# Kernel optimization log

Hardware: AMD Instinct MI355X
Metric: run time of the kernel (lower is better)

## Reference

```python
import math
import jax, jax.numpy as jnp
import numpy as np

# MrLoRA ranks: halving from highest_rank = total_rank//2 = 32 down to 1
RANKS = [32, 16, 8, 4, 2, 1]
TOTAL_R = sum(RANKS)  # 63
LORA_ALPHA = 16.0
IN_F, OUT_F = 4096, 4096
BATCH, SEQ = 4, 2048


def setup_inputs() -> dict:
    key = jax.random.key(0)
    k0, k1, k2, k3 = jax.random.split(key, 4)
    x = jax.random.normal(k0, (BATCH, SEQ, IN_F), dtype=jnp.float32)
    # Base linear layer (nn.Linear weight is [out, in], plus bias)
    W_base = jax.random.normal(k1, (OUT_F, IN_F), dtype=jnp.float32) * 0.02
    b_base = jnp.zeros((OUT_F,), dtype=jnp.float32)
    # Concatenated per-rank LoRA weights: A rows stacked -> [TOTAL_R, IN_F],
    # B cols stacked -> [OUT_F, TOTAL_R]. Mathematically identical to the
    # per-rank ModuleDict since the branch outputs are summed.
    A = jax.random.normal(k2, (TOTAL_R, IN_F), dtype=jnp.float32) / math.sqrt(IN_F)
    B = jax.random.normal(k3, (OUT_F, TOTAL_R), dtype=jnp.float32) * 0.02
    alphas = jnp.ones((len(RANKS),), dtype=jnp.float32)
    # use_rslora=True -> scaling = alpha / sqrt(r)
    scalings = jnp.array([LORA_ALPHA / math.sqrt(r) for r in RANKS], dtype=jnp.float32)
    return {"x": x, "W_base": W_base, "b_base": b_base, "A": A, "B": B,
            "alphas": alphas, "scalings": scalings}


def reference(x, W_base, b_base, A, B, alphas, scalings):
    # static map: row r of concatenated A belongs to which rank branch
    seg = np.repeat(np.arange(len(RANKS)), RANKS)  # [TOTAL_R]
    base = jnp.einsum('bsi,oi->bso', x, W_base) + b_base
    # dropout p=0 -> identity
    combined = (alphas * scalings)[seg]            # [TOTAL_R]
    z = jnp.einsum('bsi,ri->bsr', x, A) * combined # scaled low-rank projections
    adapter = jnp.einsum('bsr,or->bso', z, B)      # sum over all rank branches
    return base + adapter
```

## Files before the change

### kernel.cpp

```cpp
#include <hip/hip_runtime.h>
#include <hip/hip_fp16.h>
#include <cstdint>

#define IN_F 4096
#define OUT_F 4096
#define M_TOT 8192
#define TOTAL_R 63

typedef __attribute__((ext_vector_type(8))) _Float16 f16x8;
typedef __attribute__((ext_vector_type(4))) float f32x4;
typedef __attribute__((ext_vector_type(8))) unsigned short u16x8;
typedef __attribute__((ext_vector_type(4))) unsigned short u16x4;

__device__ __forceinline__ void gload_lds16(const void* g, void* l) {
  __builtin_amdgcn_global_load_lds((const __attribute__((address_space(1))) void*)g,
                                   (__attribute__((address_space(3))) void*)l,
                                   16, 0, 0);
}

__device__ __forceinline__ int seg_of(int r) {
  return (r < 32) ? 0 : (r < 48) ? 1 : (r < 56) ? 2 : (r < 60) ? 3 : (r < 62) ? 4 : 5;
}

__global__ void conv_x_f16(const float* __restrict__ x, uint16_t* __restrict__ xh) {
  size_t i = (size_t)blockIdx.x * blockDim.x + threadIdx.x;
  const float4* xv = (const float4*)x;
  float4 v0 = xv[2 * i];
  float4 v1 = xv[2 * i + 1];
  float v[8] = {v0.x, v0.y, v0.z, v0.w, v1.x, v1.y, v1.z, v1.w};
  u16x8 h;
#pragma unroll
  for (int k = 0; k < 8; ++k) h[k] = __half_as_ushort(__float2half_rn(v[k]));
  *(u16x8*)(xh + 8 * i) = h;
}

__global__ __launch_bounds__(256) void merge_w_kernel(
    const float* __restrict__ Wb, const float* __restrict__ A,
    const float* __restrict__ Bm, const float* __restrict__ alphas,
    const float* __restrict__ scalings, uint16_t* __restrict__ wh) {
  __shared__ float sA[63 * 256];
  __shared__ float sBT[63 * 64];
  const int t = threadIdx.x;
  const int bo = blockIdx.x >> 4, bi = blockIdx.x & 15;
  const int o0 = bo * 64, i0 = bi * 256;
  const int wv = t >> 6, ln = t & 63;

#pragma unroll
  for (int k = 0; k < 16; ++k) {
    int r = k * 4 + wv;
    if (r < 63) {
      f32x4 v = *(const f32x4*)(A + (size_t)r * IN_F + i0 + ln * 4);
      *(f32x4*)(sA + r * 256 + ln * 4) = v;
    }
  }
  {
    const int oo = ln;
    const int rbase = wv * 16;
#pragma unroll
    for (int rr = 0; rr < 16; ++rr) {
      int r = rbase + rr;
      if (r < 63) {
        int s = seg_of(r);
        sBT[r * 64 + oo] = Bm[(size_t)(o0 + oo) * TOTAL_R + r] * alphas[s] * scalings[s];
      }
    }
  }
  __syncthreads();

  const int oo = t & 63, iq = t >> 6;
  const size_t obase = (size_t)(o0 + oo) * IN_F + i0 + iq * 64;
  f32x4 acc4[16];
#pragma unroll
  for (int v = 0; v < 16; ++v) acc4[v] = *(const f32x4*)(Wb + obase + v * 4);
#pragma unroll 9
  for (int r = 0; r < 63; ++r) {
    const float coeff = sBT[r * 64 + oo];
    const f32x4* ar = (const f32x4*)(sA + r * 256 + iq * 64);
#pragma unroll
    for (int v = 0; v < 16; ++v) acc4[v] += coeff * ar[v];
  }
#pragma unroll
  for (int v = 0; v < 16; ++v) {
    u16x4 h;
#pragma unroll
    for (int k = 0; k < 4; ++k) h[k] = __half_as_ushort(__float2half_rn(acc4[v][k]));
    *(u16x4*)(wh + obase + v * 4) = h;
  }
}

__global__ __launch_bounds__(256, 2) void gemm_mrlora(
    const uint16_t* __restrict__ xh, const uint16_t* __restrict__ wh,
    const float* __restrict__ bias, float* __restrict__ out) {
  __shared__ uint16_t sX[8192];
  __shared__ uint16_t sW[4096];
  const int t = threadIdx.x;
  const int l = t & 63;
  const int w = t >> 6;
  const int wr = w >> 1, wc = w & 1;
  const int lr = l & 15, lg = l >> 4;

  const int xcd = blockIdx.x & 7;
  const int kk = blockIdx.x >> 3;
  const int bm = xcd * 4 + (kk & 3);
  const int bn = kk >> 2;
  const size_t brow = (size_t)bm * 256;
  const size_t bcol = (size_t)bn * 128;

  const int lrow = t >> 3;
  const int sp = (t & 7) ^ (lrow & 7);
  const int grow = lrow * 2 + (sp >> 2);
  const int gcol = (sp & 3) * 8;
  const uint16_t* pX = xh + (brow + grow) * (size_t)IN_F + gcol;
  const uint16_t* pW = wh + (bcol + grow) * (size_t)IN_F + gcol;
  const int t8 = t * 8;

  int aoff[8], boff[4];
#pragma unroll
  for (int i = 0; i < 8; ++i) {
    int row = wr * 128 + i * 16 + lr;
    aoff[i] = (row >> 1) * 64 + (((((row & 1) << 2) | lg) ^ ((row >> 1) & 7)) << 3);
  }
#pragma unroll
  for (int j = 0; j < 4; ++j) {
    int row = wc * 64 + j * 16 + lr;
    boff[j] = (row >> 1) * 64 + (((((row & 1) << 2) | lg) ^ ((row >> 1) & 7)) << 3);
  }

  f32x4 acc[8][4] = {};

  for (int kt = 0; kt < IN_F / 32; ++kt) {
    const int k0 = kt * 32;
#pragma unroll
    for (int g = 0; g < 4; ++g)
      gload_lds16(pX + (size_t)(64 * g) * IN_F + k0, &sX[t8 + g * 2048]);
#pragma unroll
    for (int g = 0; g < 2; ++g)
      gload_lds16(pW + (size_t)(64 * g) * IN_F + k0, &sW[t8 + g * 2048]);
    __syncthreads();

    f16x8 af[8], bf[4];
#pragma unroll
    for (int i = 0; i < 8; ++i) af[i] = *(const f16x8*)&sX[aoff[i]];
#pragma unroll
    for (int j = 0; j < 4; ++j) bf[j] = *(const f16x8*)&sW[boff[j]];

#pragma unroll
    for (int i = 0; i < 8; ++i)
#pragma unroll
      for (int j = 0; j < 4; ++j)
        acc[i][j] = __builtin_amdgcn_mfma_f32_16x16x32_f16(af[i], bf[j], acc[i][j], 0, 0, 0);

    __syncthreads();
  }

#pragma unroll
  for (int j = 0; j < 4; ++j) {
    const size_t col = bcol + wc * 64 + j * 16 + lr;
    const float bs = bias[col];
#pragma unroll
    for (int i = 0; i < 8; ++i) {
      const size_t row0 = brow + wr * 128 + i * 16 + lg * 4;
#pragma unroll
      for (int r = 0; r < 4; ++r)
        out[(row0 + r) * OUT_F + col] = acc[i][j][r] + bs;
    }
  }
}


__global__ __launch_bounds__(256) void fb_z_kernel(const float* __restrict__ x,
                                                   const float* __restrict__ A,
                                                   const float* __restrict__ alphas,
                                                   const float* __restrict__ scalings,
                                                   float* __restrict__ z) {
  __shared__ float sx[IN_F];
  __shared__ float red[256];
  const int m = blockIdx.x, t = threadIdx.x;
  for (int i = t; i < IN_F / 4; i += 256)
    ((float4*)sx)[i] = ((const float4*)(x + (size_t)m * IN_F))[i];
  __syncthreads();
  const int r = t >> 2, q = t & 3;
  float part = 0.f;
  if (r < TOTAL_R) {
    const float4* Ar = (const float4*)(A + (size_t)r * IN_F + q * 1024);
    const float4* xs = (const float4*)(sx + q * 1024);
    for (int k = 0; k < 256; ++k) {
      float4 av = Ar[k], xv = xs[k];
      part += av.x * xv.x + av.y * xv.y + av.z * xv.z + av.w * xv.w;
    }
  }
  red[t] = part;
  __syncthreads();
  if (q == 0 && r < TOTAL_R) {
    int s = seg_of(r);
    z[(size_t)m * TOTAL_R + r] =
        alphas[s] * scalings[s] * (red[t] + red[t + 1] + red[t + 2] + red[t + 3]);
  }
}

__global__ __launch_bounds__(256) void fb_gemm_fp32(const float* __restrict__ x,
                                                    const float* __restrict__ Wb,
                                                    const float* __restrict__ bb,
                                                    const float* __restrict__ Bm,
                                                    const float* __restrict__ z,
                                                    float* __restrict__ out) {
  __shared__ float sx[64][33];
  __shared__ float sw[64][33];
  const int t = threadIdx.x;
  const int tr = t >> 4, tc = t & 15;
  const int bm = blockIdx.x / (OUT_F / 64);
  const int bn = blockIdx.x % (OUT_F / 64);
  const size_t brow = (size_t)bm * 64, bcol = (size_t)bn * 64;
  const int r = t >> 2, c0 = (t & 3) * 8;
  float acc[4][4] = {};
  for (int k0 = 0; k0 < IN_F; k0 += 32) {
    float4 a0 = *(const float4*)(x + (brow + r) * IN_F + k0 + c0);
    float4 a1 = *(const float4*)(x + (brow + r) * IN_F + k0 + c0 + 4);
    float4 w0 = *(const float4*)(Wb + (bcol + r) * IN_F + k0 + c0);
    float4 w1 = *(const float4*)(Wb + (bcol + r) * IN_F + k0 + c0 + 4);
    __syncthreads();
    sx[r][c0 + 0] = a0.x; sx[r][c0 + 1] = a0.y; sx[r][c0 + 2] = a0.z; sx[r][c0 + 3] = a0.w;
    sx[r][c0 + 4] = a1.x; sx[r][c0 + 5] = a1.y; sx[r][c0 + 6] = a1.z; sx[r][c0 + 7] = a1.w;
    sw[r][c0 + 0] = w0.x; sw[r][c0 + 1] = w0.y; sw[r][c0 + 2] = w0.z; sw[r][c0 + 3] = w0.w;
    sw[r][c0 + 4] = w1.x; sw[r][c0 + 5] = w1.y; sw[r][c0 + 6] = w1.z; sw[r][c0 + 7] = w1.w;
    __syncthreads();
#pragma unroll
    for (int k = 0; k < 32; ++k) {
      float xa[4], wv[4];
#pragma unroll
      for (int i = 0; i < 4; ++i) xa[i] = sx[tr + 16 * i][k];
#pragma unroll
      for (int j = 0; j < 4; ++j) wv[j] = sw[tc + 16 * j][k];
#pragma unroll
      for (int i = 0; i < 4; ++i)
#pragma unroll
        for (int j = 0; j < 4; ++j) acc[i][j] += xa[i] * wv[j];
    }
  }
#pragma unroll 1
  for (int rr = 0; rr < TOTAL_R; ++rr) {
    float zr[4], br[4];
#pragma unroll
    for (int i = 0; i < 4; ++i) zr[i] = z[(brow + tr + 16 * i) * TOTAL_R + rr];
#pragma unroll
    for (int j = 0; j < 4; ++j) br[j] = Bm[(bcol + tc + 16 * j) * TOTAL_R + rr];
#pragma unroll
    for (int i = 0; i < 4; ++i)
#pragma unroll
      for (int j = 0; j < 4; ++j) acc[i][j] += zr[i] * br[j];
  }
#pragma unroll
  for (int i = 0; i < 4; ++i)
#pragma unroll
    for (int j = 0; j < 4; ++j) {
      size_t row = brow + tr + 16 * i, col = bcol + tc + 16 * j;
      out[row * OUT_F + col] = acc[i][j] + bb[col];
    }
}

extern "C" void kernel_launch(void* const* d_in, const int* in_sizes, int n_in,
                              void* d_out, int out_size, void* d_ws, size_t ws_size,
                              hipStream_t stream) {
  const float* x  = (const float*)d_in[0];
  const float* Wb = (const float*)d_in[1];
  const float* bb = (const float*)d_in[2];
  const float* A  = (const float*)d_in[3];
  const float* Bm = (const float*)d_in[4];
  const float* al = (const float*)d_in[5];
  const float* sc = (const float*)d_in[6];
  float* out = (float*)d_out;

  const size_t MB = (size_t)1 << 20;
  if (ws_size >= 96 * MB) {
    char* ws = (char*)d_ws;
    uint16_t* xh = (uint16_t*)(ws);
    uint16_t* wh = (uint16_t*)(ws + 64 * MB);
    conv_x_f16<<<(M_TOT * IN_F / 8) / 256, 256, 0, stream>>>(x, xh);
    merge_w_kernel<<<(OUT_F / 64) * (IN_F / 256), 256, 0, stream>>>(Wb, A, Bm, al, sc, wh);
    gemm_mrlora<<<(M_TOT / 256) * (OUT_F / 128), 256, 0, stream>>>(xh, wh, bb, out);
  } else {
    float* z = (float*)d_ws;
    fb_z_kernel<<<M_TOT, 256, 0, stream>>>(x, A, al, sc, z);
    fb_gemm_fp32<<<(M_TOT / 64) * (OUT_F / 64), 256, 0, stream>>>(x, Wb, bb, Bm, z, out);
  }
}
```

Measured before the change: 404.9 us.

## Double-buffer LDS tiles in fused GEMM to overlap global loads with MFMA

Splits the shared-memory X and W tiles into two buffers and prefetches the next K-slice with global_load_lds while the current slice is consumed by MFMAs. Partial vmcnt waits and raw s_barrier replace the two __syncthreads per iteration, and s_setprio raises wave priority around the MFMA block. This is meant to hide global load latency that was exposed each iteration. It doubles LDS use to 48KB, drops the minimum-2-blocks launch bound, and may lower occupancy. It also relies on the vmcnt(6) count matching the six loads issued per stage.

```diff
diff --git a/kernel.cpp b/kernel.cpp
--- a/kernel.cpp
+++ b/kernel.cpp
@@ -88,11 +88,11 @@
   }
 }
 
-__global__ __launch_bounds__(256, 2) void gemm_mrlora(
+__global__ __launch_bounds__(256) void gemm_mrlora(
     const uint16_t* __restrict__ xh, const uint16_t* __restrict__ wh,
     const float* __restrict__ bias, float* __restrict__ out) {
-  __shared__ uint16_t sX[8192];
-  __shared__ uint16_t sW[4096];
+  __shared__ uint16_t sX[2][8192];
+  __shared__ uint16_t sW[2][4096];
   const int t = threadIdx.x;
   const int l = t & 63;
   const int w = t >> 6;
@@ -128,30 +128,45 @@
 
   f32x4 acc[8][4] = {};
 
+#define STAGE(buf, ktv)                                                        \
+  do {                                                                         \
+    const int _k0 = (ktv) * 32;                                                \
+    _Pragma("unroll") for (int g = 0; g < 4; ++g)                              \
+      gload_lds16(pX + (size_t)(64 * g) * IN_F + _k0, &sX[buf][t8 + g * 2048]);\
+    _Pragma("unroll") for (int g = 0; g < 2; ++g)                              \
+      gload_lds16(pW + (size_t)(64 * g) * IN_F + _k0, &sW[buf][t8 + g * 2048]);\
+  } while (0)
+
+  STAGE(0, 0);
   for (int kt = 0; kt < IN_F / 32; ++kt) {
-    const int k0 = kt * 32;
-#pragma unroll
-    for (int g = 0; g < 4; ++g)
-      gload_lds16(pX + (size_t)(64 * g) * IN_F + k0, &sX[t8 + g * 2048]);
-#pragma unroll
-    for (int g = 0; g < 2; ++g)
-      gload_lds16(pW + (size_t)(64 * g) * IN_F + k0, &sW[t8 + g * 2048]);
-    __syncthreads();
+    const int cur = kt & 1;
+    if (kt + 1 < IN_F / 32) {
+      STAGE(cur ^ 1, kt + 1);
+      asm volatile("s_waitcnt vmcnt(6)" ::: "memory");
+    } else {
+      asm volatile("s_waitcnt vmcnt(0)" ::: "memory");
+    }
+    __builtin_amdgcn_s_barrier();
+    __builtin_amdgcn_sched_barrier(0);
 
     f16x8 af[8], bf[4];
 #pragma unroll
-    for (int i = 0; i < 8; ++i) af[i] = *(const f16x8*)&sX[aoff[i]];
-#pragma unroll
-    for (int j = 0; j < 4; ++j) bf[j] = *(const f16x8*)&sW[boff[j]];
-
+    for (int i = 0; i < 8; ++i) af[i] = *(const f16x8*)&sX[cur][aoff[i]];
+#pragma unroll
+    for (int j = 0; j < 4; ++j) bf[j] = *(const f16x8*)&sW[cur][boff[j]];
+
+    __builtin_amdgcn_s_setprio(1);
 #pragma unroll
     for (int i = 0; i < 8; ++i)
 #pragma unroll
       for (int j = 0; j < 4; ++j)
         acc[i][j] = __builtin_amdgcn_mfma_f32_16x16x32_f16(af[i], bf[j], acc[i][j], 0, 0, 0);
-
-    __syncthreads();
-  }
+    __builtin_amdgcn_s_setprio(0);
+
+    __builtin_amdgcn_sched_barrier(0);
+    __builtin_amdgcn_s_barrier();
+  }
+#undef STAGE
 
 #pragma unroll
   for (int j = 0; j < 4; ++j) {
```

Result: slower. 429.7 us (+6.1%).
